# Kernel optimization log

Hardware: AMD Instinct MI355X
Metric: run time of the kernel (lower is better)

## Reference

```python
import jax, jax.numpy as jnp
import numpy as np

S = 4  # HMM states
# allowed transitions among the 4 recurrent states (plus self-loops);
# the (0,4) edge targets a terminal state outside the recurrent block and is omitted
_allow = np.zeros((S, S), dtype=bool)
for i, j in [(0, 0), (1, 1), (2, 2), (3, 3), (0, 1), (1, 2), (2, 3), (0, 2), (1, 3)]:
    _allow[i, j] = True
MASK = jnp.asarray(_allow)
NEG = -1e9


def setup_inputs() -> dict:
    key = jax.random.key(0)
    k0, k1, k2, k3, k4 = jax.random.split(key, 5)
    return {
        "x": jax.random.normal(k0, (256, 4096, 26), dtype=jnp.float32),
        "emit_logits": jax.random.normal(k1, (S, 26), dtype=jnp.float32) * 0.3,
        "trans_logits": jax.random.normal(k2, (S, S), dtype=jnp.float32) * 0.3,
        "init_logits": jax.random.normal(k3, (S,), dtype=jnp.float32) * 0.3,
        "w_out": jax.random.normal(k4, (1, S, 5), dtype=jnp.float32) * 0.3,
    }


def _posterior(x, emit_logits, trans_logits, init_logits):
    # x: [B,T,A] logits -> softmax over alphabet (as in call())
    p = jax.nn.softmax(x, axis=-1)                       # [B,T,A]
    Bmat = jax.nn.softmax(emit_logits, axis=-1)          # [S,A] emission distributions
    # expected emission likelihood per state, in log space
    log_emit = jnp.log(jnp.einsum('bta,sa->bts', p, Bmat) + 1e-16)  # [B,T,S]

    neg = jnp.asarray(NEG, x.dtype)
    logA = jax.nn.log_softmax(jnp.where(MASK, trans_logits, neg), axis=-1)
    logA = jnp.where(MASK, logA, neg)                    # [S,S]
    log_pi = jax.nn.log_softmax(init_logits)             # [S]

    le = jnp.moveaxis(log_emit, 1, 0)                    # [T,B,S]
    T = le.shape[0]

    # forward recursion: alpha_t = e_t + LSE_prev(alpha_{t-1} + logA)
    a0 = log_pi[None, :] + le[0]                         # [B,S]
    def fstep(carry, e):
        nc = e + jax.nn.logsumexp(carry[:, :, None] + logA[None], axis=1)
        return nc, nc
    _, alphas = jax.lax.scan(fstep, a0, le[1:])
    alphas = jnp.concatenate([a0[None], alphas], axis=0)  # [T,B,S]

    # backward recursion: beta_t = LSE_next(logA + e_{t+1} + beta_{t+1})
    bT = jnp.zeros_like(a0)
    def bstep(carry, e_next):
        nc = jax.nn.logsumexp(logA[None] + (e_next + carry)[:, None, :], axis=2)
        return nc, nc
    _, betas = jax.lax.scan(bstep, bT, le[1:], reverse=True)
    betas = jnp.concatenate([betas, bT[None]], axis=0)    # [T,B,S]

    gamma = jax.nn.softmax(alphas + betas, axis=-1)       # posterior [T,B,S]
    return jnp.moveaxis(gamma, 0, 1)[:, :, None, :]       # [B,T,1,S]


def reference(x, emit_logits, trans_logits, init_logits, w_out):
    gamma = _posterior(x, emit_logits, trans_logits, init_logits)  # [B,T,1,S]
    return jnp.einsum('bthd,hdo->bto', gamma, w_out)               # [B,T,5]
```

## Files before the change

kernel.cpp:

```cpp
#include <hip/hip_runtime.h>

#define TDIM 4096
#define BDIM 256
#define ADIM 26
#define SDIM 4
#define LOG2E 1.44269504088896340736f

__device__ __forceinline__ float ex2(float x) { return __builtin_amdgcn_exp2f(x); }
__device__ __forceinline__ float rcp(float x) { return __builtin_amdgcn_rcpf(x); }

struct TransA { float A00, A01, A02, A11, A12, A13, A22, A23, A33; };

__device__ __forceinline__ TransA make_transA(const float* __restrict__ trans) {
    TransA A;
    {
        float l0 = trans[0], l1 = trans[1], l2 = trans[2];
        float m = fmaxf(fmaxf(l0, l1), l2);
        float e0 = __expf(l0 - m), e1 = __expf(l1 - m), e2 = __expf(l2 - m);
        float s = 1.f / (e0 + e1 + e2);
        A.A00 = e0 * s; A.A01 = e1 * s; A.A02 = e2 * s;
    }
    {
        float l1 = trans[5], l2 = trans[6], l3 = trans[7];
        float m = fmaxf(fmaxf(l1, l2), l3);
        float e1 = __expf(l1 - m), e2 = __expf(l2 - m), e3 = __expf(l3 - m);
        float s = 1.f / (e1 + e2 + e3);
        A.A11 = e1 * s; A.A12 = e2 * s; A.A13 = e3 * s;
    }
    {
        float l2 = trans[10], l3 = trans[11];
        float m = fmaxf(l2, l3);
        float e2 = __expf(l2 - m), e3 = __expf(l3 - m);
        float s = 1.f / (e2 + e3);
        A.A22 = e2 * s; A.A23 = e3 * s;
    }
    A.A33 = 1.f;
    return A;
}

struct UT { float m00, m01, m02, m03, m11, m12, m13, m22, m23, m33; };

__device__ __forceinline__ void fstep(UT& M, const TransA& A, float4 e) {
    float n00 = M.m00 * A.A00 * e.x;
    float n01 = fmaf(M.m00, A.A01, M.m01 * A.A11) * e.y;
    float n02 = fmaf(M.m00, A.A02, fmaf(M.m01, A.A12, M.m02 * A.A22)) * e.z;
    float n03 = fmaf(M.m01, A.A13, fmaf(M.m02, A.A23, M.m03)) * e.w;
    float n11 = M.m11 * A.A11 * e.y;
    float n12 = fmaf(M.m11, A.A12, M.m12 * A.A22) * e.z;
    float n13 = fmaf(M.m11, A.A13, fmaf(M.m12, A.A23, M.m13)) * e.w;
    float n22 = M.m22 * A.A22 * e.z;
    float n23 = fmaf(M.m22, A.A23, M.m23) * e.w;
    float n33 = M.m33 * e.w;
    float m1 = fmaxf(fmaxf(n00, n01), fmaxf(n02, n03));
    float m2 = fmaxf(fmaxf(n11, n12), fmaxf(n13, n22));
    float s = rcp(fmaxf(fmaxf(m1, m2), fmaxf(n23, n33)));
    M.m00 = n00 * s; M.m01 = n01 * s; M.m02 = n02 * s; M.m03 = n03 * s;
    M.m11 = n11 * s; M.m12 = n12 * s; M.m13 = n13 * s;
    M.m22 = n22 * s; M.m23 = n23 * s; M.m33 = n33 * s;
}

__device__ __forceinline__ UT ut_compose(const UT& A, const UT& B) {
    UT C;
    C.m00 = A.m00 * B.m00;
    C.m01 = fmaf(A.m00, B.m01, A.m01 * B.m11);
    C.m02 = fmaf(A.m00, B.m02, fmaf(A.m01, B.m12, A.m02 * B.m22));
    C.m03 = fmaf(A.m00, B.m03, fmaf(A.m01, B.m13, fmaf(A.m02, B.m23, A.m03 * B.m33)));
    C.m11 = A.m11 * B.m11;
    C.m12 = fmaf(A.m11, B.m12, A.m12 * B.m22);
    C.m13 = fmaf(A.m11, B.m13, fmaf(A.m12, B.m23, A.m13 * B.m33));
    C.m22 = A.m22 * B.m22;
    C.m23 = fmaf(A.m22, B.m23, A.m23 * B.m33);
    C.m33 = A.m33 * B.m33;
    return C;
}

__device__ __forceinline__ void ut_renorm(UT& M) {
    float m1 = fmaxf(fmaxf(M.m00, M.m01), fmaxf(M.m02, M.m03));
    float m2 = fmaxf(fmaxf(M.m11, M.m12), fmaxf(M.m13, M.m22));
    float s = rcp(fmaxf(fmaxf(m1, m2), fmaxf(M.m23, M.m33)));
    M.m00 *= s; M.m01 *= s; M.m02 *= s; M.m03 *= s;
    M.m11 *= s; M.m12 *= s; M.m13 *= s; M.m22 *= s; M.m23 *= s; M.m33 *= s;
}

__device__ __forceinline__ void ut_store11(float* p, const UT& M) {
    p[0] = M.m00; p[1] = M.m01; p[2] = M.m02; p[3] = M.m03;
    p[4] = M.m11; p[5] = M.m12; p[6] = M.m13;
    p[7] = M.m22; p[8] = M.m23; p[9] = M.m33;
}
__device__ __forceinline__ UT ut_load11(const float* p) {
    UT M;
    M.m00 = p[0]; M.m01 = p[1]; M.m02 = p[2]; M.m03 = p[3];
    M.m11 = p[4]; M.m12 = p[5]; M.m13 = p[6];
    M.m22 = p[7]; M.m23 = p[8]; M.m33 = p[9];
    return M;
}

__device__ __forceinline__ void vecmat(float& v0, float& v1, float& v2, float& v3,
                                       const float* m) {
    float n0 = v0 * m[0];
    float n1 = fmaf(v0, m[1], v1 * m[4]);
    float n2 = fmaf(v0, m[2], fmaf(v1, m[5], v2 * m[7]));
    float n3 = fmaf(v0, m[3], fmaf(v1, m[6], fmaf(v2, m[8], v3 * m[9])));
    float s = rcp(fmaxf(fmaxf(n0, n1), fmaxf(n2, n3)));
    v0 = n0 * s; v1 = n1 * s; v2 = n2 * s; v3 = n3 * s;
}
__device__ __forceinline__ void matvec(const float* m,
                                       float& u0, float& u1, float& u2, float& u3) {
    float n0 = fmaf(m[0], u0, fmaf(m[1], u1, fmaf(m[2], u2, m[3] * u3)));
    float n1 = fmaf(m[4], u1, fmaf(m[5], u2, m[6] * u3));
    float n2 = fmaf(m[7], u2, m[8] * u3);
    float n3 = m[9] * u3;
    float s = rcp(fmaxf(fmaxf(n0, n1), fmaxf(n2, n3)));
    u0 = n0 * s; u1 = n1 * s; u2 = n2 * s; u3 = n3 * s;
}

#define ASTEP(E) do { \
    float4 _e = (E); \
    float n0_ = a0 * A.A00 * _e.x; \
    float n1_ = fmaf(a0, A.A01, a1 * A.A11) * _e.y; \
    float n2_ = fmaf(a0, A.A02, fmaf(a1, A.A12, a2 * A.A22)) * _e.z; \
    float n3_ = fmaf(a1, A.A13, fmaf(a2, A.A23, a3)) * _e.w; \
    float s_ = rcp(fmaxf(fmaxf(n0_, n1_), fmaxf(n2_, n3_))); \
    a0 = n0_ * s_; a1 = n1_ * s_; a2 = n2_ * s_; a3 = n3_ * s_; \
} while (0)

#define BSTEP(E) do { \
    float4 _e = (E); \
    float f0_ = _e.x * b0, f1_ = _e.y * b1, f2_ = _e.z * b2, f3_ = _e.w * b3; \
    float n0_ = fmaf(A.A00, f0_, fmaf(A.A01, f1_, A.A02 * f2_)); \
    float n1_ = fmaf(A.A11, f1_, fmaf(A.A12, f2_, A.A13 * f3_)); \
    float n2_ = fmaf(A.A22, f2_, A.A23 * f3_); \
    float n3_ = f3_; \
    float s_ = rcp(fmaxf(fmaxf(n0_, n1_), fmaxf(n2_, n3_))); \
    b0 = n0_ * s_; b1 = n1_ * s_; b2 = n2_ * s_; b3 = n3_ * s_; \
} while (0)

#define GEMIT(AV, Q) do { \
    float g0_ = (AV).x * b0, g1_ = (AV).y * b1, g2_ = (AV).z * b2, g3_ = (AV).w * b3; \
    float inv_ = rcp(g0_ + g1_ + g2_ + g3_); \
    float q0_ = g0_ * inv_, q1_ = g1_ * inv_, q2_ = g2_ * inv_, q3_ = g3_ * inv_; \
    vals[(Q)*5 + 0] = fmaf(q0_, wv[0][0], fmaf(q1_, wv[1][0], fmaf(q2_, wv[2][0], q3_ * wv[3][0]))); \
    vals[(Q)*5 + 1] = fmaf(q0_, wv[0][1], fmaf(q1_, wv[1][1], fmaf(q2_, wv[2][1], q3_ * wv[3][1]))); \
    vals[(Q)*5 + 2] = fmaf(q0_, wv[0][2], fmaf(q1_, wv[1][2], fmaf(q2_, wv[2][2], q3_ * wv[3][2]))); \
    vals[(Q)*5 + 3] = fmaf(q0_, wv[0][3], fmaf(q1_, wv[1][3], fmaf(q2_, wv[2][3], q3_ * wv[3][3]))); \
    vals[(Q)*5 + 4] = fmaf(q0_, wv[0][4], fmaf(q1_, wv[1][4], fmaf(q2_, wv[2][4], q3_ * wv[3][4]))); \
} while (0)

#define RDLE(T) sle[(((T) & 15) * 257) + ((T) >> 4)]

#define L0F 0
#define L0B 2816
#define L1F 5632
#define L1B 7040
#define L2F 8448
#define L2B 9152
#define L3F 9856
#define L3B 10208
#define SF  10560
#define SB  10688

__global__ __launch_bounds__(512, 1)
void fused_kernel(const float* __restrict__ x, const float* __restrict__ emit,
                  const float* __restrict__ trans, const float* __restrict__ initl,
                  const float* __restrict__ w, float* __restrict__ out) {
    __shared__ float4 sle[16 * 257];
    __shared__ float4 uni[4096];
    __shared__ float Bmat[SDIM][ADIM];

    float* U = reinterpret_cast<float*>(uni);
    float4* abuf = uni;
    float4* bbuf = uni + 2048;

    const int tid = threadIdx.x;
    const int bidb = blockIdx.x;

    if (tid < SDIM) {
        float m = -1e30f;
        #pragma unroll
        for (int a = 0; a < ADIM; ++a) m = fmaxf(m, emit[tid * ADIM + a]);
        float tmp[ADIM];
        float z = 0.f;
        #pragma unroll
        for (int a = 0; a < ADIM; ++a) {
            float e = __expf(emit[tid * ADIM + a] - m);
            tmp[a] = e; z += e;
        }
        float inv = 1.f / z;
        #pragma unroll
        for (int a = 0; a < ADIM; ++a) Bmat[tid][a] = tmp[a] * inv;
    }
    TransA A = make_transA(trans);
    __syncthreads();

    {
        const float4* xbase = reinterpret_cast<const float4*>(x) + (size_t)bidb * 2048 * 13;
        #pragma unroll 1
        for (int i = 0; i < 4; ++i) {
            const float4* xp = xbase + ((size_t)(i * 512 + tid)) * 13;
            float4 buf[13];
            #pragma unroll
            for (int q = 0; q < 13; ++q) buf[q] = xp[q];

            float d00 = 0.f, d01 = 0.f, d02 = 0.f, d03 = 0.f;
            float d10 = 0.f, d11 = 0.f, d12 = 0.f, d13 = 0.f;
            #pragma unroll
            for (int q = 0; q < 13; ++q) {
                float4 u = buf[q];
                #pragma unroll
                for (int j = 0; j < 4; ++j) {
                    const int e = q * 4 + j;
                    float val = (j == 0) ? u.x : (j == 1) ? u.y : (j == 2) ? u.z : u.w;
                    float ev = ex2(val * LOG2E);
                    if (e < ADIM) {
                        d00 = fmaf(ev, Bmat[0][e], d00); d01 = fmaf(ev, Bmat[1][e], d01);
                        d02 = fmaf(ev, Bmat[2][e], d02); d03 = fmaf(ev, Bmat[3][e], d03);
                    } else {
                        const int a = e - ADIM;
                        d10 = fmaf(ev, Bmat[0][a], d10); d11 = fmaf(ev, Bmat[1][a], d11);
                        d12 = fmaf(ev, Bmat[2][a], d12); d13 = fmaf(ev, Bmat[3][a], d13);
                    }
                }
            }
            int t = (i * 512 + tid) << 1;
            RDLE(t) = make_float4(d00, d01, d02, d03);
            RDLE(t + 1) = make_float4(d10, d11, d12, d13);
        }
    }
    __syncthreads();

    const int c = tid & 255;
    const int t0 = c * 16;
    const bool isB = tid >= 256;

    {
        UT M;
        if (!isB) {
            float4 e0 = RDLE(t0);
            if (c == 0) {
                M.m00 = e0.x; M.m11 = e0.y; M.m22 = e0.z; M.m33 = e0.w;
                M.m01 = 0.f; M.m02 = 0.f; M.m03 = 0.f; M.m12 = 0.f; M.m13 = 0.f; M.m23 = 0.f;
            } else {
                M.m00 = A.A00 * e0.x; M.m01 = A.A01 * e0.y; M.m02 = A.A02 * e0.z; M.m03 = 0.f;
                M.m11 = A.A11 * e0.y; M.m12 = A.A12 * e0.z; M.m13 = A.A13 * e0.w;
                M.m22 = A.A22 * e0.z; M.m23 = A.A23 * e0.w; M.m33 = e0.w;
            }
            #pragma unroll 1
            for (int k = 1; k < 16; ++k) fstep(M, A, RDLE(t0 + k));
            ut_renorm(M);
            ut_store11(U + L0F + c * 11, M);
        } else {
            M.m00 = 1.f; M.m11 = 1.f; M.m22 = 1.f; M.m33 = 1.f;
            M.m01 = 0.f; M.m02 = 0.f; M.m03 = 0.f; M.m12 = 0.f; M.m13 = 0.f; M.m23 = 0.f;
            int nst = (c == 255) ? 15 : 16;
            #pragma unroll 1
            for (int k = 0; k < nst; ++k) fstep(M, A, RDLE(t0 + 1 + k));
            ut_renorm(M);
            ut_store11(U + L0B + c * 11, M);
        }
    }
    __syncthreads();

    if (tid < 256) {
        int dir = tid >> 7;
        int i = tid & 127;
        const float* src = U + (dir ? L0B : L0F);
        float* dst = U + (dir ? L1B : L1F);
        UT P = ut_compose(ut_load11(src + (2 * i) * 11), ut_load11(src + (2 * i + 1) * 11));
        ut_renorm(P);
        ut_store11(dst + i * 11, P);
    }
    __syncthreads();

    if (tid < 128) {
        int dir = tid >> 6;
        int i = tid & 63;
        const float* src = U + (dir ? L1B : L1F);
        float* dst = U + (dir ? L2B : L2F);
        UT P = ut_compose(ut_load11(src + (2 * i) * 11), ut_load11(src + (2 * i + 1) * 11));
        ut_renorm(P);
        ut_store11(dst + i * 11, P);
    }
    __syncthreads();

    if (tid < 64) {
        int dir = tid >> 5;
        int i = tid & 31;
        const float* src = U + (dir ? L2B : L2F);
        float* dst = U + (dir ? L3B : L3F);
        UT P = ut_compose(ut_load11(src + (2 * i) * 11), ut_load11(src + (2 * i + 1) * 11));
        ut_renorm(P);
        ut_store11(dst + i * 11, P);
    }
    __syncthreads();

    if (tid == 0) {
        float i0 = initl[0], i1 = initl[1], i2 = initl[2], i3 = initl[3];
        float m = fmaxf(fmaxf(i0, i1), fmaxf(i2, i3));
        float e0 = __expf(i0 - m), e1 = __expf(i1 - m), e2 = __expf(i2 - m), e3 = __expf(i3 - m);
        float s = 1.f / (e0 + e1 + e2 + e3);
        float v0 = e0 * s, v1 = e1 * s, v2 = e2 * s, v3 = e3 * s;
        #pragma unroll 1
        for (int g = 0; g < 32; ++g) {
            U[SF + g * 4 + 0] = v0; U[SF + g * 4 + 1] = v1;
            U[SF + g * 4 + 2] = v2; U[SF + g * 4 + 3] = v3;
            vecmat(v0, v1, v2, v3, U + L3F + g * 11);
        }
    } else if (tid == 64) {
        float u0 = 1.f, u1 = 1.f, u2 = 1.f, u3 = 1.f;
        #pragma unroll 1
        for (int g = 31; g >= 0; --g) {
            U[SB + g * 4 + 0] = u0; U[SB + g * 4 + 1] = u1;
            U[SB + g * 4 + 2] = u2; U[SB + g * 4 + 3] = u3;
            matvec(U + L3B + g * 11, u0, u1, u2, u3);
        }
    }
    __syncthreads();

    float fa0, fa1, fa2, fa3;
    float fb0, fb1, fb2, fb3;
    {
        int g = c >> 3;
        if (!isB) {
            fa0 = U[SF + g * 4 + 0]; fa1 = U[SF + g * 4 + 1];
            fa2 = U[SF + g * 4 + 2]; fa3 = U[SF + g * 4 + 3];
            if (c & 4) vecmat(fa0, fa1, fa2, fa3, U + L2F + (2 * g) * 11);
            if (c & 2) vecmat(fa0, fa1, fa2, fa3, U + L1F + ((c >> 2) * 2) * 11);
            if (c & 1) vecmat(fa0, fa1, fa2, fa3, U + L0F + (c - 1) * 11);
        } else {
            fb0 = U[SB + g * 4 + 0]; fb1 = U[SB + g * 4 + 1];
            fb2 = U[SB + g * 4 + 2]; fb3 = U[SB + g * 4 + 3];
            if (!(c & 4)) matvec(U + L2B + (2 * g + 1) * 11, fb0, fb1, fb2, fb3);
            if (!(c & 2)) matvec(U + L1B + ((c >> 2) * 2 + 1) * 11, fb0, fb1, fb2, fb3);
            if (!(c & 1)) matvec(U + L0B + (c + 1) * 11, fb0, fb1, fb2, fb3);
        }
    }
    __syncthreads();

    float wv[SDIM][5];
    #pragma unroll
    for (int s = 0; s < SDIM; ++s)
        #pragma unroll
        for (int o = 0; o < 5; ++o) wv[s][o] = w[s * 5 + o];

    float* opb = out + (size_t)bidb * TDIM * 5;
    float vals[20];

    if (!isB) {
        float a0 = fa0, a1 = fa1, a2 = fa2, a3 = fa3;
        if (c == 0) {
            float4 e = RDLE(0);
            float n0 = a0 * e.x, n1 = a1 * e.y, n2 = a2 * e.z, n3 = a3 * e.w;
            float s = rcp(fmaxf(fmaxf(n0, n1), fmaxf(n2, n3)));
            a0 = n0 * s; a1 = n1 * s; a2 = n2 * s; a3 = n3 * s;
        } else {
            ASTEP(RDLE(t0));
        }
        abuf[0 * 256 + c] = make_float4(a0, a1, a2, a3);
        #pragma unroll 1
        for (int k = 1; k < 8; ++k) {
            ASTEP(RDLE(t0 + k));
            abuf[k * 256 + c] = make_float4(a0, a1, a2, a3);
        }
        __syncthreads();
        float b0, b1, b2, b3;
        #pragma unroll 1
        for (int g2 = 0; g2 < 2; ++g2) {
            #pragma unroll
            for (int q = 0; q < 4; ++q) {
                int k = 8 + g2 * 4 + q;
                ASTEP(RDLE(t0 + k));
                float4 bv = bbuf[(k - 8) * 256 + c];
                b0 = bv.x; b1 = bv.y; b2 = bv.z; b3 = bv.w;
                float4 av = make_float4(a0, a1, a2, a3);
                GEMIT(av, q);
            }
            float4* vo = reinterpret_cast<float4*>(opb + (size_t)(t0 + 8 + g2 * 4) * 5);
            vo[0] = make_float4(vals[0],  vals[1],  vals[2],  vals[3]);
            vo[1] = make_float4(vals[4],  vals[5],  vals[6],  vals[7]);
            vo[2] = make_float4(vals[8],  vals[9],  vals[10], vals[11]);
            vo[3] = make_float4(vals[12], vals[13], vals[14], vals[15]);
            vo[4] = make_float4(vals[16], vals[17], vals[18], vals[19]);
        }
    } else {
        float b0 = fb0, b1 = fb1, b2 = fb2, b3 = fb3;
        bool lastc = (c == 255);
        #pragma unroll 1
        for (int k = 15; k >= 8; --k) {
            if (!(lastc && k == 15)) BSTEP(RDLE(t0 + 1 + k));
            bbuf[(k - 8) * 256 + c] = make_float4(b0, b1, b2, b3);
        }
        __syncthreads();
        #pragma unroll 1
        for (int g2 = 1; g2 >= 0; --g2) {
            #pragma unroll
            for (int q = 3; q >= 0; --q) {
                int k = g2 * 4 + q;
                BSTEP(RDLE(t0 + 1 + k));
                float4 av = abuf[k * 256 + c];
                GEMIT(av, q);
            }
            float4* vo = reinterpret_cast<float4*>(opb + (size_t)(t0 + g2 * 4) * 5);
            vo[0] = make_float4(vals[0],  vals[1],  vals[2],  vals[3]);
            vo[1] = make_float4(vals[4],  vals[5],  vals[6],  vals[7]);
            vo[2] = make_float4(vals[8],  vals[9],  vals[10], vals[11]);
            vo[3] = make_float4(vals[12], vals[13], vals[14], vals[15]);
            vo[4] = make_float4(vals[16], vals[17], vals[18], vals[19]);
        }
    }
}

extern "C" void kernel_launch(void* const* d_in, const int* in_sizes, int n_in,
                              void* d_out, int out_size, void* d_ws, size_t ws_size,
                              hipStream_t stream) {
    const float* x     = (const float*)d_in[0];
    const float* emit  = (const float*)d_in[1];
    const float* trans = (const float*)d_in[2];
    const float* initl = (const float*)d_in[3];
    const float* w     = (const float*)d_in[4];
    float* out = (float*)d_out;

    hipLaunchKernelGGL(fused_kernel, dim3(BDIM), dim3(512), 0, stream,
                       x, emit, trans, initl, w, out);
}
```

Baseline: 40.38 us.

## Give each thread an 8-step chunk running both forward and backward passes

Each of the 512 threads now owns an 8-timestep chunk and computes both the forward and backward chunk transfer matrices, instead of 256 threads per direction each owning 16 steps. The scan tree gains one more level, and the final alpha/beta sweeps keep their values in registers rather than exchanging halves through shared memory, which removes a barrier and the LDS staging buffers. The aim is to halve the serial chain length per thread and cut shared-memory traffic. The cost is more register pressure from the arrays, an extra tree level, and both fstep chains interleaved in one thread.

```diff
diff --git a/kernel.cpp b/kernel.cpp
--- a/kernel.cpp
+++ b/kernel.cpp
@@ -146,30 +146,30 @@
     vals[(Q)*5 + 4] = fmaf(q0_, wv[0][4], fmaf(q1_, wv[1][4], fmaf(q2_, wv[2][4], q3_ * wv[3][4]))); \
 } while (0)
 
-#define RDLE(T) sle[(((T) & 15) * 257) + ((T) >> 4)]
+#define RDLE(T) sle[(((T) & 7) * 513) + ((T) >> 3)]
 
 #define L0F 0
-#define L0B 2816
-#define L1F 5632
-#define L1B 7040
-#define L2F 8448
-#define L2B 9152
-#define L3F 9856
-#define L3B 10208
-#define SF  10560
-#define SB  10688
+#define L0B 5632
+#define L1F 11264
+#define L1B 14080
+#define L2F 16896
+#define L2B 18304
+#define L3F 19712
+#define L3B 20416
+#define L4F 21120
+#define L4B 21472
+#define SF  21824
+#define SB  21952
 
 __global__ __launch_bounds__(512, 1)
 void fused_kernel(const float* __restrict__ x, const float* __restrict__ emit,
                   const float* __restrict__ trans, const float* __restrict__ initl,
                   const float* __restrict__ w, float* __restrict__ out) {
-    __shared__ float4 sle[16 * 257];
-    __shared__ float4 uni[4096];
+    __shared__ float4 sle[8 * 513];
+    __shared__ float4 uni[5520];
     __shared__ float Bmat[SDIM][ADIM];
 
     float* U = reinterpret_cast<float*>(uni);
-    float4* abuf = uni;
-    float4* bbuf = uni + 2048;
 
     const int tid = threadIdx.x;
     const int bidb = blockIdx.x;
@@ -228,41 +228,38 @@
     }
     __syncthreads();
 
-    const int c = tid & 255;
-    const int t0 = c * 16;
-    const bool isB = tid >= 256;
-
-    {
-        UT M;
-        if (!isB) {
-            float4 e0 = RDLE(t0);
-            if (c == 0) {
-                M.m00 = e0.x; M.m11 = e0.y; M.m22 = e0.z; M.m33 = e0.w;
-                M.m01 = 0.f; M.m02 = 0.f; M.m03 = 0.f; M.m12 = 0.f; M.m13 = 0.f; M.m23 = 0.f;
-            } else {
-                M.m00 = A.A00 * e0.x; M.m01 = A.A01 * e0.y; M.m02 = A.A02 * e0.z; M.m03 = 0.f;
-                M.m11 = A.A11 * e0.y; M.m12 = A.A12 * e0.z; M.m13 = A.A13 * e0.w;
-                M.m22 = A.A22 * e0.z; M.m23 = A.A23 * e0.w; M.m33 = e0.w;
-            }
-            #pragma unroll 1
-            for (int k = 1; k < 16; ++k) fstep(M, A, RDLE(t0 + k));
-            ut_renorm(M);
-            ut_store11(U + L0F + c * 11, M);
+    const int c = tid;
+    const int t0 = c * 8;
+
+    {
+        UT Mf, Mb;
+        float4 e0 = RDLE(t0);
+        if (c == 0) {
+            Mf.m00 = e0.x; Mf.m11 = e0.y; Mf.m22 = e0.z; Mf.m33 = e0.w;
+            Mf.m01 = 0.f; Mf.m02 = 0.f; Mf.m03 = 0.f; Mf.m12 = 0.f; Mf.m13 = 0.f; Mf.m23 = 0.f;
         } else {
-            M.m00 = 1.f; M.m11 = 1.f; M.m22 = 1.f; M.m33 = 1.f;
-            M.m01 = 0.f; M.m02 = 0.f; M.m03 = 0.f; M.m12 = 0.f; M.m13 = 0.f; M.m23 = 0.f;
-            int nst = (c == 255) ? 15 : 16;
-            #pragma unroll 1
-            for (int k = 0; k < nst; ++k) fstep(M, A, RDLE(t0 + 1 + k));
-            ut_renorm(M);
-            ut_store11(U + L0B + c * 11, M);
-        }
-    }
-    __syncthreads();
-
-    if (tid < 256) {
-        int dir = tid >> 7;
-        int i = tid & 127;
+            Mf.m00 = A.A00 * e0.x; Mf.m01 = A.A01 * e0.y; Mf.m02 = A.A02 * e0.z; Mf.m03 = 0.f;
+            Mf.m11 = A.A11 * e0.y; Mf.m12 = A.A12 * e0.z; Mf.m13 = A.A13 * e0.w;
+            Mf.m22 = A.A22 * e0.z; Mf.m23 = A.A23 * e0.w; Mf.m33 = e0.w;
+        }
+        Mb.m00 = 1.f; Mb.m11 = 1.f; Mb.m22 = 1.f; Mb.m33 = 1.f;
+        Mb.m01 = 0.f; Mb.m02 = 0.f; Mb.m03 = 0.f; Mb.m12 = 0.f; Mb.m13 = 0.f; Mb.m23 = 0.f;
+
+        #pragma unroll 1
+        for (int k = 1; k < 8; ++k) {
+            float4 e = RDLE(t0 + k);
+            fstep(Mf, A, e);
+            fstep(Mb, A, e);
+        }
+        if (c < 511) fstep(Mb, A, RDLE(t0 + 8));
+        ut_renorm(Mf); ut_renorm(Mb);
+        ut_store11(U + L0F + c * 11, Mf);
+        ut_store11(U + L0B + c * 11, Mb);
+    }
+    __syncthreads();
+
+    {
+        int dir = tid >> 8, i = tid & 255;
         const float* src = U + (dir ? L0B : L0F);
         float* dst = U + (dir ? L1B : L1F);
         UT P = ut_compose(ut_load11(src + (2 * i) * 11), ut_load11(src + (2 * i + 1) * 11));
@@ -271,9 +268,8 @@
     }
     __syncthreads();
 
-    if (tid < 128) {
-        int dir = tid >> 6;
-        int i = tid & 63;
+    if (tid < 256) {
+        int dir = tid >> 7, i = tid & 127;
         const float* src = U + (dir ? L1B : L1F);
         float* dst = U + (dir ? L2B : L2F);
         UT P = ut_compose(ut_load11(src + (2 * i) * 11), ut_load11(src + (2 * i + 1) * 11));
@@ -282,11 +278,20 @@
     }
     __syncthreads();
 
-    if (tid < 64) {
-        int dir = tid >> 5;
-        int i = tid & 31;
+    if (tid < 128) {
+        int dir = tid >> 6, i = tid & 63;
         const float* src = U + (dir ? L2B : L2F);
         float* dst = U + (dir ? L3B : L3F);
+        UT P = ut_compose(ut_load11(src + (2 * i) * 11), ut_load11(src + (2 * i + 1) * 11));
+        ut_renorm(P);
+        ut_store11(dst + i * 11, P);
+    }
+    __syncthreads();
+
+    if (tid < 64) {
+        int dir = tid >> 5, i = tid & 31;
+        const float* src = U + (dir ? L3B : L3F);
+        float* dst = U + (dir ? L4B : L4F);
         UT P = ut_compose(ut_load11(src + (2 * i) * 11), ut_load11(src + (2 * i + 1) * 11));
         ut_renorm(P);
         ut_store11(dst + i * 11, P);
@@ -303,7 +308,7 @@
         for (int g = 0; g < 32; ++g) {
             U[SF + g * 4 + 0] = v0; U[SF + g * 4 + 1] = v1;
             U[SF + g * 4 + 2] = v2; U[SF + g * 4 + 3] = v3;
-            vecmat(v0, v1, v2, v3, U + L3F + g * 11);
+            vecmat(v0, v1, v2, v3, U + L4F + g * 11);
         }
     } else if (tid == 64) {
         float u0 = 1.f, u1 = 1.f, u2 = 1.f, u3 = 1.f;
@@ -311,7 +316,7 @@
         for (int g = 31; g >= 0; --g) {
             U[SB + g * 4 + 0] = u0; U[SB + g * 4 + 1] = u1;
             U[SB + g * 4 + 2] = u2; U[SB + g * 4 + 3] = u3;
-            matvec(U + L3B + g * 11, u0, u1, u2, u3);
+            matvec(U + L4B + g * 11, u0, u1, u2, u3);
         }
     }
     __syncthreads();
@@ -319,22 +324,21 @@
     float fa0, fa1, fa2, fa3;
     float fb0, fb1, fb2, fb3;
     {
-        int g = c >> 3;
-        if (!isB) {
-            fa0 = U[SF + g * 4 + 0]; fa1 = U[SF + g * 4 + 1];
-            fa2 = U[SF + g * 4 + 2]; fa3 = U[SF + g * 4 + 3];
-            if (c & 4) vecmat(fa0, fa1, fa2, fa3, U + L2F + (2 * g) * 11);
-            if (c & 2) vecmat(fa0, fa1, fa2, fa3, U + L1F + ((c >> 2) * 2) * 11);
-            if (c & 1) vecmat(fa0, fa1, fa2, fa3, U + L0F + (c - 1) * 11);
-        } else {
-            fb0 = U[SB + g * 4 + 0]; fb1 = U[SB + g * 4 + 1];
-            fb2 = U[SB + g * 4 + 2]; fb3 = U[SB + g * 4 + 3];
-            if (!(c & 4)) matvec(U + L2B + (2 * g + 1) * 11, fb0, fb1, fb2, fb3);
-            if (!(c & 2)) matvec(U + L1B + ((c >> 2) * 2 + 1) * 11, fb0, fb1, fb2, fb3);
-            if (!(c & 1)) matvec(U + L0B + (c + 1) * 11, fb0, fb1, fb2, fb3);
-        }
-    }
-    __syncthreads();
+        int g = c >> 4;
+        fa0 = U[SF + g * 4 + 0]; fa1 = U[SF + g * 4 + 1];
+        fa2 = U[SF + g * 4 + 2]; fa3 = U[SF + g * 4 + 3];
+        if (c & 8) vecmat(fa0, fa1, fa2, fa3, U + L3F + (2 * g) * 11);
+        if (c & 4) vecmat(fa0, fa1, fa2, fa3, U + L2F + ((c >> 3) * 2) * 11);
+        if (c & 2) vecmat(fa0, fa1, fa2, fa3, U + L1F + ((c >> 2) * 2) * 11);
+        if (c & 1) vecmat(fa0, fa1, fa2, fa3, U + L0F + (c - 1) * 11);
+
+        fb0 = U[SB + g * 4 + 0]; fb1 = U[SB + g * 4 + 1];
+        fb2 = U[SB + g * 4 + 2]; fb3 = U[SB + g * 4 + 3];
+        if (!(c & 8)) matvec(U + L3B + (2 * g + 1) * 11, fb0, fb1, fb2, fb3);
+        if (!(c & 4)) matvec(U + L2B + ((c >> 3) * 2 + 1) * 11, fb0, fb1, fb2, fb3);
+        if (!(c & 2)) matvec(U + L1B + ((c >> 2) * 2 + 1) * 11, fb0, fb1, fb2, fb3);
+        if (!(c & 1)) matvec(U + L0B + (c + 1) * 11, fb0, fb1, fb2, fb3);
+    }
 
     float wv[SDIM][5];
     #pragma unroll
@@ -343,61 +347,42 @@
         for (int o = 0; o < 5; ++o) wv[s][o] = w[s * 5 + o];
 
     float* opb = out + (size_t)bidb * TDIM * 5;
-    float vals[20];
-
-    if (!isB) {
+
+    float4 br[8];
+    {
+        float b0 = fb0, b1 = fb1, b2 = fb2, b3 = fb3;
+        #pragma unroll
+        for (int k = 7; k >= 0; --k) {
+            if (!(c == 511 && k == 7)) BSTEP(RDLE(t0 + 1 + k));
+            br[k] = make_float4(b0, b1, b2, b3);
+        }
+    }
+    float4 ar[8];
+    {
         float a0 = fa0, a1 = fa1, a2 = fa2, a3 = fa3;
-        if (c == 0) {
-            float4 e = RDLE(0);
-            float n0 = a0 * e.x, n1 = a1 * e.y, n2 = a2 * e.z, n3 = a3 * e.w;
-            float s = rcp(fmaxf(fmaxf(n0, n1), fmaxf(n2, n3)));
-            a0 = n0 * s; a1 = n1 * s; a2 = n2 * s; a3 = n3 * s;
-        } else {
-            ASTEP(RDLE(t0));
-        }
-        abuf[0 * 256 + c] = make_float4(a0, a1, a2, a3);
-        #pragma unroll 1
-        for (int k = 1; k < 8; ++k) {
-            ASTEP(RDLE(t0 + k));
-            abuf[k * 256 + c] = make_float4(a0, a1, a2, a3);
-        }
-        __syncthreads();
+        #pragma unroll
+        for (int k = 0; k < 8; ++k) {
+            if (c == 0 && k == 0) {
+                float4 e = RDLE(0);
+                float n0 = a0 * e.x, n1 = a1 * e.y, n2 = a2 * e.z, n3 = a3 * e.w;
+                float s = rcp(fmaxf(fmaxf(n0, n1), fmaxf(n2, n3)));
+                a0 = n0 * s; a1 = n1 * s; a2 = n2 * s; a3 = n3 * s;
+            } else {
+                ASTEP(RDLE(t0 + k));
+            }
+            ar[k] = make_float4(a0, a1, a2, a3);
+        }
+    }
+    {
+        float vals[20];
         float b0, b1, b2, b3;
-        #pragma unroll 1
+        #pragma unroll
         for (int g2 = 0; g2 < 2; ++g2) {
             #pragma unroll
             for (int q = 0; q < 4; ++q) {
-                int k = 8 + g2 * 4 + q;
-                ASTEP(RDLE(t0 + k));
-                float4 bv = bbuf[(k - 8) * 256 + c];
-                b0 = bv.x; b1 = bv.y; b2 = bv.z; b3 = bv.w;
-                float4 av = make_float4(a0, a1, a2, a3);
-                GEMIT(av, q);
-            }
-            float4* vo = reinterpret_cast<float4*>(opb + (size_t)(t0 + 8 + g2 * 4) * 5);
-            vo[0] = make_float4(vals[0],  vals[1],  vals[2],  vals[3]);
-            vo[1] = make_float4(vals[4],  vals[5],  vals[6],  vals[7]);
-            vo[2] = make_float4(vals[8],  vals[9],  vals[10], vals[11]);
-            vo[3] = make_float4(vals[12], vals[13], vals[14], vals[15]);
-            vo[4] = make_float4(vals[16], vals[17], vals[18], vals[19]);
-        }
-    } else {
-        float b0 = fb0, b1 = fb1, b2 = fb2, b3 = fb3;
-        bool lastc = (c == 255);
-        #pragma unroll 1
-        for (int k = 15; k >= 8; --k) {
-            if (!(lastc && k == 15)) BSTEP(RDLE(t0 + 1 + k));
-            bbuf[(k - 8) * 256 + c] = make_float4(b0, b1, b2, b3);
-        }
-        __syncthreads();
-        #pragma unroll 1
-        for (int g2 = 1; g2 >= 0; --g2) {
-            #pragma unroll
-            for (int q = 3; q >= 0; --q) {
                 int k = g2 * 4 + q;
-                BSTEP(RDLE(t0 + 1 + k));
-                float4 av = abuf[k * 256 + c];
-                GEMIT(av, q);
+                b0 = br[k].x; b1 = br[k].y; b2 = br[k].z; b3 = br[k].w;
+                GEMIT(ar[k], q);
             }
             float4* vo = reinterpret_cast<float4*>(opb + (size_t)(t0 + g2 * 4) * 5);
             vo[0] = make_float4(vals[0],  vals[1],  vals[2],  vals[3]);
```

New measurement: 39.34 us. 1.03x faster.
